# Kernel optimization log

Measured on AMD Instinct MI355X. Metric: run time of the kernel, lower is better.

The kernel has to match this reference:

```python
import jax, jax.numpy as jnp
import numpy as np

N_NODES = 50000
N_EDGES = 1600000
HIDDEN = 256
N_GRAPHS = 1024
N_PROPS = 8
N_FEAT = 4
IN_DIM = N_FEAT + 4 * 8 + 4 * 8  # 68


def setup_inputs() -> dict:
    key = jax.random.key(0)
    ks = jax.random.split(key, 20)
    s = 0.05
    inp = {
        "x": jax.random.randint(ks[0], (N_NODES, N_FEAT), 0, 720),
        "edge_index": jax.random.randint(ks[1], (2, N_EDGES), 0, N_NODES),
        "batch": jnp.sort(jax.random.randint(ks[2], (N_NODES,), 0, N_GRAPHS)),
        "emb24": jax.random.normal(ks[3], (24, 8), jnp.float32) * s,
        "emb72": jax.random.normal(ks[4], (72, 8), jnp.float32) * s,
        "lin1_w": jax.random.normal(ks[5], (HIDDEN, IN_DIM), jnp.float32) * s,
        "lin1_b": jnp.zeros((HIDDEN,), jnp.float32),
        "qa1_w": jax.random.normal(ks[6], (HIDDEN, HIDDEN), jnp.float32) * s,
        "qa1_b": jnp.zeros((HIDDEN,), jnp.float32),
        "lin2_w": jax.random.normal(ks[7], (HIDDEN, HIDDEN), jnp.float32) * s,
        "lin2_b": jnp.zeros((HIDDEN,), jnp.float32),
        "qa2_w": jax.random.normal(ks[8], (HIDDEN, HIDDEN), jnp.float32) * s,
        "qa2_b": jnp.zeros((HIDDEN,), jnp.float32),
        "head_w1": jax.random.normal(ks[9], (N_PROPS, HIDDEN // 2, HIDDEN), jnp.float32) * s,
        "head_b1": jnp.zeros((N_PROPS, HIDDEN // 2), jnp.float32),
        "head_w2": jax.random.normal(ks[10], (N_PROPS, 1, HIDDEN // 2), jnp.float32) * s,
        "head_b2": jnp.zeros((N_PROPS, 1), jnp.float32),
    }
    return inp


def _qagcn_conv(h, src, dst, lin_w, lin_b, qa_w, qa_b):
    n = h.shape[0]
    lin_x = h @ lin_w.T + lin_b                                  # [N, H]
    # message = lin(x_j); aggr='add' over edges; add_self_loops contributes
    # one extra lin_x per node, and update() adds lin(x) again -> 2*lin_x.
    aggr = jax.ops.segment_sum(lin_x[src], dst, num_segments=n)  # [N, H]
    h2 = aggr + 2.0 * lin_x
    b, e, _, _ = jnp.split(h2, 4, axis=-1)
    h3 = jnp.concatenate([b, e, b + e, b + 2.0 * e], axis=-1)
    return jax.nn.relu(h3 @ qa_w.T + qa_b)


def reference(x, edge_index, batch, emb24, emb72, lin1_w, lin1_b, qa1_w, qa1_b,
              lin2_w, lin2_b, qa2_w, qa2_b, head_w1, head_b1, head_w2, head_b2):
    n = x.shape[0]
    r24 = emb24[x % 24].reshape(n, -1)          # [N, 32]
    r72 = emb72[x % 72].reshape(n, -1)          # [N, 32]
    h = jnp.concatenate([x.astype(jnp.float32), r24, r72], axis=-1)  # [N, 68]
    src, dst = edge_index[0], edge_index[1]
    h = _qagcn_conv(h, src, dst, lin1_w, lin1_b, qa1_w, qa1_b)
    h = _qagcn_conv(h, src, dst, lin2_w, lin2_b, qa2_w, qa2_b)
    # global mean pool over graphs
    sums = jax.ops.segment_sum(h, batch, num_segments=N_GRAPHS)      # [G, H]
    cnts = jax.ops.segment_sum(jnp.ones((n,), h.dtype), batch, num_segments=N_GRAPHS)
    g = sums / jnp.maximum(cnts, 1.0)[:, None]                       # [G, H]
    # per-property 2-layer MLP heads
    h1 = jax.nn.relu(jnp.einsum('gd,phd->pgh', g, head_w1) + head_b1[:, None, :])
    out = jnp.einsum('pgh,poh->pgo', h1, head_w2) + head_b2[:, None, :]  # [P, G, 1]
    return out[..., 0].T                                             # [G, P]
```

## Files before the change

kernel.cpp:

```cpp
#include <hip/hip_runtime.h>
#include <hip/hip_bf16.h>

#define N_NODESC 50000
#define N_EDGESC 1600000
#define NGC 1024
#define NPC 8
#define NBIN 196
#define NBLKE 391

typedef __attribute__((ext_vector_type(8))) short bf16x8;
typedef __attribute__((ext_vector_type(4))) float f32x4;

__device__ inline ushort f2bf(float f) {
  union { float f; uint u; } v; v.f = f;
  uint u = v.u;
  u += 0x7FFF + ((u >> 16) & 1);
  return (ushort)(u >> 16);
}
__device__ inline float bflo(uint u) {
  union { uint u; float f; } v; v.u = u << 16; return v.f;
}
__device__ inline float bfhi(uint u) {
  union { uint u; float f; } v; v.u = u & 0xFFFF0000u; return v.f;
}

__global__ __launch_bounds__(256) void megaprep(
    const float* __restrict__ qa1w, const float* __restrict__ qa2w,
    const float* __restrict__ lin1w, const float* __restrict__ lin2w,
    ushort* __restrict__ qe1, ushort* __restrict__ qe2,
    ushort* __restrict__ l1w, ushort* __restrict__ l2w,
    const int* __restrict__ x, const float* __restrict__ e24,
    const float* __restrict__ e72, ushort* __restrict__ feat,
    const int* __restrict__ dst, int* __restrict__ bh) {
  int bid = blockIdx.x, t = threadIdx.x;
  if (bid < 256) {
    const float* qw = (bid < 128) ? qa1w : qa2w;
    ushort* eff = (bid < 128) ? qe1 : qe2;
    int k = (bid & 127) * 2 + (t >> 7);
    int j = t & 127;
    const float* r = qw + (size_t)k * 256;
    float v;
    if (j < 64) v = r[j] + r[128 + j] + r[192 + j];
    else { int j2 = j - 64; v = r[64 + j2] + r[128 + j2] + 2.0f * r[192 + j2]; }
    eff[(size_t)k * 128 + j] = f2bf(v);
  } else if (bid < 304) {
    int i = (bid - 256) * 256 + t;
    int r = i / 96, c = i - r * 96;
    l1w[i] = (c < 68) ? f2bf(lin1w[(size_t)r * 68 + c]) : (ushort)0;
  } else if (bid < 432) {
    int r = bid - 304;
    l2w[(size_t)r * 256 + t] = f2bf(lin2w[(size_t)r * 256 + t]);
  } else if (bid < 1456) {
    const int stride = 1024 * 256;
    for (int i = (bid - 432) * 256 + t; i < N_NODESC * 96; i += stride) {
      int n = i / 96, tt = i - n * 96;
      float v = 0.f;
      if (tt < 4) v = (float)x[n * 4 + tt];
      else if (tt < 36) { int kk = tt - 4;  int f = kk >> 3, c = kk & 7; v = e24[(x[n * 4 + f] % 24) * 8 + c]; }
      else if (tt < 68) { int kk = tt - 36; int f = kk >> 3, c = kk & 7; v = e72[(x[n * 4 + f] % 72) * 8 + c]; }
      feat[i] = f2bf(v);
    }
  } else {
    __shared__ int hist[NBIN];
    int blk = bid - 1456;
    if (t < NBIN) hist[t] = 0;
    __syncthreads();
    int base = blk * 4096;
#pragma unroll
    for (int i = 0; i < 16; ++i) {
      int idx = base + i * 256 + t;
      if (idx < N_EDGESC) atomicAdd(&hist[dst[idx] >> 8], 1);
    }
    __syncthreads();
    if (t < NBIN) bh[(size_t)t * NBLKE + blk] = hist[t];
  }
}

__global__ __launch_bounds__(64) void csr_scan_bins(int* __restrict__ bh, int* __restrict__ bt) {
  int bin = blockIdx.x;
  int lane = threadIdx.x;
  int carry = 0;
  int* row = bh + (size_t)bin * NBLKE;
  for (int c = 0; c < NBLKE; c += 64) {
    int j = c + lane;
    int v = (j < NBLKE) ? row[j] : 0;
    int incl = v;
#pragma unroll
    for (int off = 1; off < 64; off <<= 1) {
      int u = __shfl_up(incl, off, 64);
      if (lane >= off) incl += u;
    }
    if (j < NBLKE) row[j] = carry + incl - v;
    carry += __shfl(incl, 63, 64);
  }
  if (lane == 0) bt[bin] = carry;
}

template <int K>
__device__ __forceinline__ void gemm_body(ushort* ws, int bx, int by,
    const ushort* __restrict__ A, const ushort* __restrict__ W,
    const float* __restrict__ bias, ushort* __restrict__ C,
    int M, int NC, int relu) {
  int tid = threadIdx.x;
  int lane = tid & 63;
  int wv = tid >> 6;
  int rbase = bx * 128 + wv * 32;
  int colt = by * 128;
  int r16 = lane & 15;
  int kg = (lane >> 4) * 8;

  const char* wt = (const char*)(W + (size_t)colt * K);
#pragma unroll
  for (int i = 0; i < K / 16; ++i) {
    int o = (i * 256 + tid) * 16;
    int col = o / (2 * K);
    int sw = o ^ ((col & 7) << 4);
    *(bf16x8*)((char*)ws + sw) = *(const bf16x8*)(wt + o);
  }
  __syncthreads();

  f32x4 acc[2][8];
#pragma unroll
  for (int m = 0; m < 2; ++m)
#pragma unroll
    for (int n = 0; n < 8; ++n) acc[m][n] = (f32x4){0.f, 0.f, 0.f, 0.f};

  for (int k0 = 0; k0 < K; k0 += 32) {
    int ks = k0 + kg;
    bf16x8 a[2], b[8];
#pragma unroll
    for (int m = 0; m < 2; ++m) {
      int rr = rbase + m * 16 + r16;
      if (rr >= M) rr = M - 1;
      a[m] = *(const bf16x8*)(A + (size_t)rr * K + ks);
    }
#pragma unroll
    for (int n = 0; n < 8; ++n) {
      int cl = n * 16 + r16;
      int byte = (cl * 2 * K + ks * 2) ^ ((cl & 7) << 4);
      b[n] = *(const bf16x8*)((const char*)ws + byte);
    }
#pragma unroll
    for (int m = 0; m < 2; ++m)
#pragma unroll
      for (int n = 0; n < 8; ++n)
        acc[m][n] = __builtin_amdgcn_mfma_f32_16x16x32_bf16(a[m], b[n], acc[m][n], 0, 0, 0);
  }

  int rowoff = (lane >> 4) * 4;
#pragma unroll
  for (int m = 0; m < 2; ++m) {
#pragma unroll
    for (int j = 0; j < 4; ++j) {
      int row = rbase + m * 16 + rowoff + j;
      if (row >= M) continue;
#pragma unroll
      for (int n = 0; n < 8; ++n) {
        int col = colt + n * 16 + r16;
        float v = acc[m][n][j] + bias[col];
        if (relu) v = fmaxf(v, 0.f);
        C[(size_t)row * NC + col] = f2bf(v);
      }
    }
  }
}

template <int K>
__global__ __launch_bounds__(256, 2) void mfma_gemm_lds(
    const ushort* __restrict__ A, const ushort* __restrict__ W,
    const float* __restrict__ bias, ushort* __restrict__ C,
    int M, int NC, int relu) {
  __shared__ ushort ws[128 * K];
  gemm_body<K>(ws, blockIdx.x, blockIdx.y, A, W, bias, C, M, NC, relu);
}

__global__ __launch_bounds__(256, 2) void scatter_lin1(
    const int* __restrict__ src, const int* __restrict__ dst,
    const int* __restrict__ bh, const int* __restrict__ bt, uint* __restrict__ tmp,
    const ushort* __restrict__ feat, const ushort* __restrict__ l1w,
    const float* __restrict__ lin1b, ushort* __restrict__ linx) {
  __shared__ ushort ws[128 * 96];
  int bid = blockIdx.x, t = threadIdx.x;
  if (bid < NBLKE) {
    int* sc = (int*)ws;
    int* cur = sc + 256;
    int v = (t < NBIN) ? bt[t] : 0;
    sc[t] = v;
    __syncthreads();
    for (int off = 1; off < 256; off <<= 1) {
      int u = (t >= off) ? sc[t - off] : 0;
      __syncthreads();
      sc[t] += u;
      __syncthreads();
    }
    if (t < NBIN) cur[t] = (sc[t] - v) + bh[(size_t)t * NBLKE + bid];
    __syncthreads();
    int base = bid * 4096;
#pragma unroll
    for (int i = 0; i < 16; ++i) {
      int idx = base + i * 256 + t;
      if (idx < N_EDGESC) {
        int d = dst[idx];
        uint p = ((uint)d << 16) | (uint)src[idx];
        int pos = atomicAdd(&cur[d >> 8], 1);
        tmp[pos] = p;
      }
    }
  } else {
    gemm_body<96>(ws, bid - NBLKE, 0, feat, l1w, lin1b, linx, N_NODESC, 128, 0);
  }
}

__global__ __launch_bounds__(256) void csr_bucket_sort(const uint* __restrict__ tmp,
                                                       const int* __restrict__ bt,
                                                       ushort* __restrict__ elist,
                                                       int* __restrict__ rp) {
  __shared__ int sc[256];
  __shared__ int cnt[256];
  int b = blockIdx.x, t = threadIdx.x;
  int v = (t < NBIN) ? bt[t] : 0;
  sc[t] = v;
  __syncthreads();
  for (int off = 1; off < 256; off <<= 1) {
    int u = (t >= off) ? sc[t - off] : 0;
    __syncthreads();
    sc[t] += u;
    __syncthreads();
  }
  int base = (b == 0) ? 0 : sc[b - 1];
  int end = sc[b];
  int total = sc[NBIN - 1];
  __syncthreads();
  cnt[t] = 0;
  __syncthreads();
  for (int i = base + t; i < end; i += 256)
    atomicAdd(&cnt[(tmp[i] >> 16) & 255], 1);
  __syncthreads();
  int cv = cnt[t];
  sc[t] = cv;
  __syncthreads();
  for (int off = 1; off < 256; off <<= 1) {
    int u = (t >= off) ? sc[t - off] : 0;
    __syncthreads();
    sc[t] += u;
    __syncthreads();
  }
  int excl = sc[t] - cv;
  int node = (b << 8) + t;
  if (node < N_NODESC) rp[node] = base + excl;
  if (b == NBIN - 1 && t == 0) rp[N_NODESC] = total;
  cnt[t] = base + excl;
  __syncthreads();
  for (int i = base + t; i < end; i += 256) {
    uint p = tmp[i];
    int pos = atomicAdd(&cnt[(p >> 16) & 255], 1);
    elist[pos] = (ushort)(p & 0xFFFFu);
  }
}

__global__ __launch_bounds__(256) void aggregate2(const uint* __restrict__ lx,
                                                  const int* __restrict__ rp,
                                                  const ushort* __restrict__ elist,
                                                  uint* __restrict__ h2) {
  int wv = threadIdx.x >> 6, lane = threadIdx.x & 63;
  int n = blockIdx.x * 4 + wv;
  int beg = rp[n], end = rp[n + 1];
  uint su = lx[(size_t)n * 64 + lane];
  float a0 = 2.f * bflo(su), a1 = 2.f * bfhi(su);
  int e = beg;
  for (; e + 16 <= end; e += 16) {
    uint r[16];
#pragma unroll
    for (int i = 0; i < 16; ++i) {
      int s = elist[e + i];
      r[i] = lx[(size_t)s * 64 + lane];
    }
#pragma unroll
    for (int i = 0; i < 16; ++i) { a0 += bflo(r[i]); a1 += bfhi(r[i]); }
  }
  for (; e + 4 <= end; e += 4) {
    uint r0 = lx[(size_t)elist[e] * 64 + lane];
    uint r1 = lx[(size_t)elist[e + 1] * 64 + lane];
    uint r2 = lx[(size_t)elist[e + 2] * 64 + lane];
    uint r3 = lx[(size_t)elist[e + 3] * 64 + lane];
    a0 += bflo(r0) + bflo(r1) + bflo(r2) + bflo(r3);
    a1 += bfhi(r0) + bfhi(r1) + bfhi(r2) + bfhi(r3);
  }
  for (; e < end; ++e) {
    uint r0 = lx[(size_t)elist[e] * 64 + lane];
    a0 += bflo(r0);
    a1 += bfhi(r0);
  }
  h2[(size_t)n * 64 + lane] = (uint)f2bf(a0) | ((uint)f2bf(a1) << 16);
}

__global__ __launch_bounds__(256) void pool2(const uint* __restrict__ h,
                                             const int* __restrict__ batch,
                                             float* __restrict__ g) {
  int gg = blockIdx.x;
  int t = threadIdx.x;
  int j = t & 127, rg = t >> 7;
  int lo = 0, hi = N_NODESC;
  while (lo < hi) { int mid = (lo + hi) >> 1; if (batch[mid] < gg) lo = mid + 1; else hi = mid; }
  int beg = lo;
  hi = N_NODESC;
  while (lo < hi) { int mid = (lo + hi) >> 1; if (batch[mid] < gg + 1) lo = mid + 1; else hi = mid; }
  int end = lo;
  float a0 = 0.f, a1 = 0.f;
  int n = beg + rg;
  for (; n + 2 < end; n += 4) {
    uint u = h[(size_t)n * 128 + j];
    uint u2 = h[(size_t)(n + 2) * 128 + j];
    a0 += bflo(u) + bflo(u2);
    a1 += bfhi(u) + bfhi(u2);
  }
  if (n < end) {
    uint u = h[(size_t)n * 128 + j];
    a0 += bflo(u);
    a1 += bfhi(u);
  }
  __shared__ float s0[128], s1[128];
  if (rg == 1) { s0[j] = a0; s1[j] = a1; }
  __syncthreads();
  if (rg == 0) {
    a0 += s0[j];
    a1 += s1[j];
    float cfac = fmaxf((float)(end - beg), 1.0f);
    g[(size_t)gg * 256 + 2 * j] = a0 / cfac;
    g[(size_t)gg * 256 + 2 * j + 1] = a1 / cfac;
  }
}

__global__ __launch_bounds__(128) void head_kernel(const float* __restrict__ g,
    const float* __restrict__ w1, const float* __restrict__ b1,
    const float* __restrict__ w2, const float* __restrict__ b2,
    float* __restrict__ out) {
  int p = blockIdx.y;
  int g0 = blockIdx.x * 8;
  int t = threadIdx.x;
  __shared__ float gs[8][256];
  for (int i = t; i < 8 * 256; i += 128)
    gs[i >> 8][i & 255] = g[(size_t)(g0 + (i >> 8)) * 256 + (i & 255)];
  __syncthreads();
  const float4* w4 = (const float4*)(w1 + ((size_t)p * 128 + t) * 256);
  float bv = b1[p * 128 + t];
  float acc[8];
#pragma unroll
  for (int q = 0; q < 8; ++q) acc[q] = bv;
  for (int d4 = 0; d4 < 64; ++d4) {
    float4 wv = w4[d4];
#pragma unroll
    for (int q = 0; q < 8; ++q) {
      acc[q] += gs[q][d4 * 4 + 0] * wv.x + gs[q][d4 * 4 + 1] * wv.y +
                gs[q][d4 * 4 + 2] * wv.z + gs[q][d4 * 4 + 3] * wv.w;
    }
  }
  float w2v = w2[p * 128 + t];
  __shared__ float red[2][8];
  int wave = t >> 6, lane = t & 63;
#pragma unroll
  for (int q = 0; q < 8; ++q) {
    float v = fmaxf(acc[q], 0.f) * w2v;
    for (int o = 32; o > 0; o >>= 1) v += __shfl_down(v, o, 64);
    if (lane == 0) red[wave][q] = v;
  }
  __syncthreads();
  if (t < 8) out[(size_t)(g0 + t) * 8 + p] = red[0][t] + red[1][t] + b2[p];
}

extern "C" void kernel_launch(void* const* d_in, const int* in_sizes, int n_in,
                              void* d_out, int out_size, void* d_ws, size_t ws_size,
                              hipStream_t stream) {
  const int*   x     = (const int*)d_in[0];
  const int*   ei    = (const int*)d_in[1];
  const int*   batch = (const int*)d_in[2];
  const float* emb24 = (const float*)d_in[3];
  const float* emb72 = (const float*)d_in[4];
  const float* lin1w = (const float*)d_in[5];
  const float* lin1b = (const float*)d_in[6];
  const float* qa1w  = (const float*)d_in[7];
  const float* qa1b  = (const float*)d_in[8];
  const float* lin2w = (const float*)d_in[9];
  const float* lin2b = (const float*)d_in[10];
  const float* qa2w  = (const float*)d_in[11];
  const float* qa2b  = (const float*)d_in[12];
  const float* hw1   = (const float*)d_in[13];
  const float* hb1   = (const float*)d_in[14];
  const float* hw2   = (const float*)d_in[15];
  const float* hb2   = (const float*)d_in[16];
  float* out = (float*)d_out;

  const int* srcv = ei;
  const int* dstv = ei + N_EDGESC;

  char* wsb = (char*)d_ws;
  size_t off = 0;
  auto alloc = [&](size_t b) { char* p = wsb + off; off += (b + 255) & ~(size_t)255; return p; };
  ushort* feat  = (ushort*)alloc((size_t)N_NODESC * 96 * 2);
  ushort* linx  = (ushort*)alloc((size_t)N_NODESC * 128 * 2);
  ushort* h2    = (ushort*)alloc((size_t)N_NODESC * 128 * 2);
  ushort* h     = (ushort*)alloc((size_t)N_NODESC * 256 * 2);
  float*  gbuf  = (float*)alloc((size_t)NGC * 256 * 4);
  ushort* qe1   = (ushort*)alloc(256 * 128 * 2);
  ushort* qe2   = (ushort*)alloc(256 * 128 * 2);
  ushort* l1w   = (ushort*)alloc(128 * 96 * 2);
  ushort* l2w   = (ushort*)alloc(128 * 256 * 2);
  int*    rp    = (int*)alloc((size_t)(N_NODESC + 1) * 4);
  ushort* elist = (ushort*)alloc((size_t)N_EDGESC * 2);
  int*    bh    = (int*)alloc((size_t)NBIN * NBLKE * 4);
  int*    bt    = (int*)alloc((size_t)NBIN * 4);
  uint*   tmp   = (uint*)h;

  megaprep<<<1847, 256, 0, stream>>>(qa1w, qa2w, lin1w, lin2w, qe1, qe2, l1w, l2w,
                                     x, emb24, emb72, feat, dstv, bh);
  csr_scan_bins<<<NBIN, 64, 0, stream>>>(bh, bt);

  int gm = (N_NODESC + 127) / 128;

  scatter_lin1<<<NBLKE + gm, 256, 0, stream>>>(srcv, dstv, bh, bt, tmp,
                                               feat, l1w, lin1b, linx);
  csr_bucket_sort<<<NBIN, 256, 0, stream>>>(tmp, bt, elist, rp);

  aggregate2<<<N_NODESC / 4, 256, 0, stream>>>((const uint*)linx, rp, elist, (uint*)h2);
  mfma_gemm_lds<128><<<dim3(gm, 2), 256, 0, stream>>>(h2, qe1, qa1b, h, N_NODESC, 256, 1);

  mfma_gemm_lds<256><<<dim3(gm, 1), 256, 0, stream>>>(h, l2w, lin2b, linx, N_NODESC, 128, 0);
  aggregate2<<<N_NODESC / 4, 256, 0, stream>>>((const uint*)linx, rp, elist, (uint*)h2);
  mfma_gemm_lds<128><<<dim3(gm, 2), 256, 0, stream>>>(h2, qe2, qa2b, h, N_NODESC, 256, 1);

  pool2<<<NGC, 256, 0, stream>>>((const uint*)h, batch, gbuf);
  head_kernel<<<dim3(NGC / 8, NPC), 128, 0, stream>>>(gbuf, hw1, hb1, hw2, hb2, out);
}
```

Measured before the change: 244.4 us.

## Sort per-node CSR neighbor lists in shared memory and deepen aggregation unroll

The bucket sort kernel now stages each bucket's edges in shared memory and insertion-sorts every node's source list before writing it out in one coalesced pass. Sorted neighbors are meant to improve locality and cache reuse of the gathered rows in the aggregation kernels, and the final writes become contiguous. The aggregation loop also issues 32 gathers per iteration, with an 8-wide tail, to keep more loads in flight. The shared buffer holds 10240 entries, so a bucket with more edges than that would overflow; the insertion sort is serial per thread and adds register pressure.

```diff
diff --git a/kernel.cpp b/kernel.cpp
--- a/kernel.cpp
+++ b/kernel.cpp
@@ -217,6 +217,7 @@
                                                        int* __restrict__ rp) {
   __shared__ int sc[256];
   __shared__ int cnt[256];
+  __shared__ ushort stage[10240];
   int b = blockIdx.x, t = threadIdx.x;
   int v = (t < NBIN) ? bt[t] : 0;
   sc[t] = v;
@@ -249,13 +250,26 @@
   int node = (b << 8) + t;
   if (node < N_NODESC) rp[node] = base + excl;
   if (b == NBIN - 1 && t == 0) rp[N_NODESC] = total;
-  cnt[t] = base + excl;
+  cnt[t] = excl;
   __syncthreads();
   for (int i = base + t; i < end; i += 256) {
     uint p = tmp[i];
     int pos = atomicAdd(&cnt[(p >> 16) & 255], 1);
-    elist[pos] = (ushort)(p & 0xFFFFu);
-  }
+    stage[pos] = (ushort)(p & 0xFFFFu);
+  }
+  __syncthreads();
+  if (node < N_NODESC) {
+    int st = excl, en = excl + cv;
+    for (int i = st + 1; i < en; ++i) {
+      ushort key = stage[i];
+      int j = i - 1;
+      while (j >= st && stage[j] > key) { stage[j + 1] = stage[j]; --j; }
+      stage[j + 1] = key;
+    }
+  }
+  __syncthreads();
+  int len = end - base;
+  for (int i = t; i < len; i += 256) elist[base + i] = stage[i];
 }
 
 __global__ __launch_bounds__(256) void aggregate2(const uint* __restrict__ lx,
@@ -268,23 +282,25 @@
   uint su = lx[(size_t)n * 64 + lane];
   float a0 = 2.f * bflo(su), a1 = 2.f * bfhi(su);
   int e = beg;
-  for (; e + 16 <= end; e += 16) {
-    uint r[16];
-#pragma unroll
-    for (int i = 0; i < 16; ++i) {
+  for (; e + 32 <= end; e += 32) {
+    uint r[32];
+#pragma unroll
+    for (int i = 0; i < 32; ++i) {
       int s = elist[e + i];
       r[i] = lx[(size_t)s * 64 + lane];
     }
 #pragma unroll
-    for (int i = 0; i < 16; ++i) { a0 += bflo(r[i]); a1 += bfhi(r[i]); }
-  }
-  for (; e + 4 <= end; e += 4) {
-    uint r0 = lx[(size_t)elist[e] * 64 + lane];
-    uint r1 = lx[(size_t)elist[e + 1] * 64 + lane];
-    uint r2 = lx[(size_t)elist[e + 2] * 64 + lane];
-    uint r3 = lx[(size_t)elist[e + 3] * 64 + lane];
-    a0 += bflo(r0) + bflo(r1) + bflo(r2) + bflo(r3);
-    a1 += bfhi(r0) + bfhi(r1) + bfhi(r2) + bfhi(r3);
+    for (int i = 0; i < 32; ++i) { a0 += bflo(r[i]); a1 += bfhi(r[i]); }
+  }
+  for (; e + 8 <= end; e += 8) {
+    uint r[8];
+#pragma unroll
+    for (int i = 0; i < 8; ++i) {
+      int s = elist[e + i];
+      r[i] = lx[(size_t)s * 64 + lane];
+    }
+#pragma unroll
+    for (int i = 0; i < 8; ++i) { a0 += bflo(r[i]); a1 += bfhi(r[i]); }
   }
   for (; e < end; ++e) {
     uint r0 = lx[(size_t)elist[e] * 64 + lane];
```

Measured after the change: 359.9 us. +47.2%, slower.
